# Kernel tuning notes

Hardware: AMD Instinct MI355X
Metric: run time of the kernel (lower is better)

Reference implementation:

```python
import jax, jax.numpy as jnp
import numpy as np

EPS = 1e-5

def _inorm(t, axes):
    m = t.mean(axis=axes, keepdims=True)
    v = t.var(axis=axes, keepdims=True)
    return (t - m) * jax.lax.rsqrt(v + EPS)

def setup_inputs() -> dict:
    key = jax.random.key(0)
    ks = jax.random.split(key, 7)
    b, c, d, o, h, w = 2, 128, 128, 128, 16, 16
    maxlen = 256
    return {
        "x": jax.random.normal(ks[0], (b, c, h, w), jnp.float32),
        "y": jax.random.normal(ks[1], (b, d, h, w), jnp.float32),
        "pos_emb": jax.random.normal(ks[2], (maxlen, c), jnp.float32) * 0.02,
        "w1": jax.random.normal(ks[3], (o, 2 * c + d), jnp.float32) * 0.05,
        "b1": jax.random.normal(ks[4], (o,), jnp.float32) * 0.01,
        "w2": jax.random.normal(ks[5], (o, o), jnp.float32) * 0.05,
        "b2": jax.random.normal(ks[6], (o,), jnp.float32) * 0.01,
    }

def reference(x, y, pos_emb, w1, b1, w2, b2):
    b, c, h, w = x.shape
    d = y.shape[1]
    hw = h * w
    # positional embedding: tokens = arange(hw), permute to channel-first
    pos = pos_emb[:hw].T.reshape(c, h, w)  # [c,h,w]
    x = x + pos[None]
    x = jax.nn.relu(_inorm(x, (2, 3)))
    y = jax.nn.relu(_inorm(y, (2, 3)))
    xf = x.reshape(b, c, hw)
    yf = y.reshape(b, d, hw)
    # conv1x1 over cat([x_i, x_j, y]) splits into three GEMMs (same math):
    Wi, Wj, Wy = w1[:, :c], w1[:, c:2 * c], w1[:, 2 * c:]
    A = jnp.einsum('oc,bcj->boj', Wi, xf)                    # varies along j
    B = jnp.einsum('oc,bci->boi', Wj, xf) + jnp.einsum('od,bdi->boi', Wy, yf)  # varies along i
    z = A[:, :, None, :] + B[:, :, :, None] + b1[None, :, None, None]  # [b,o,hw,hw]
    z = jax.nn.relu(_inorm(z, (2, 3)))
    # second conv1x1 then sum over dim=3 commutes: w2 @ sum_j z + hw*b2
    s = z.sum(axis=3)  # [b,o,hw]
    out = jnp.einsum('po,boi->bpi', w2, s) + hw * b2[None, :, None]
    return out.reshape(b, -1, h, w)
```

## Files before the change

### kernel.cpp

```cpp
#include <hip/hip_runtime.h>

#define HW 256
#define C  128

__device__ __forceinline__ void blockReduce4(float& a, float& b, float& c, float& d,
                                             float (*sm)[4]) {
    #pragma unroll
    for (int off = 32; off > 0; off >>= 1) {
        a += __shfl_down(a, off, 64);
        b += __shfl_down(b, off, 64);
        c += __shfl_down(c, off, 64);
        d += __shfl_down(d, off, 64);
    }
    const int wid  = threadIdx.x >> 6;
    const int lane = threadIdx.x & 63;
    if (lane == 0) { sm[wid][0] = a; sm[wid][1] = b; sm[wid][2] = c; sm[wid][3] = d; }
    __syncthreads();
    a = sm[0][0] + sm[1][0] + sm[2][0] + sm[3][0];
    b = sm[0][1] + sm[1][1] + sm[2][1] + sm[3][1];
    c = sm[0][2] + sm[1][2] + sm[2][2] + sm[3][2];
    d = sm[0][3] + sm[1][3] + sm[2][3] + sm[3][3];
}

__global__ __launch_bounds__(256) void k_norm(
        const float* __restrict__ x, const float* __restrict__ y,
        const float* __restrict__ pos, float* __restrict__ xn, float* __restrict__ yn) {
    __shared__ float sm[4][4];
    const int blk = blockIdx.x;
    const int tid = threadIdx.x;
    float v;
    float* dst;
    if (blk < 256) {
        const int c = blk & 127;
        v = x[blk * HW + tid] + pos[tid * C + c];
        dst = xn + blk * HW;
    } else {
        const int bc = blk - 256;
        v = y[bc * HW + tid];
        dst = yn + bc * HW;
    }
    float s = v, s2 = v * v, z3 = 0.0f, z4 = 0.0f;
    blockReduce4(s, s2, z3, z4, sm);
    const float m    = s  * (1.0f / 256.0f);
    const float var  = s2 * (1.0f / 256.0f) - m * m;
    const float r    = (v - m) * rsqrtf(var + 1e-5f);
    dst[tid] = r > 0.0f ? r : 0.0f;
}

__global__ __launch_bounds__(256) void k_rel(
        const float* __restrict__ xn, const float* __restrict__ yn,
        const float* __restrict__ w1, float* __restrict__ s_out) {
    __shared__ float sm[4][4];
    __shared__ float wrow[384];
    __shared__ float sha[256];
    const int bo = blockIdx.x;
    const int b  = bo >> 7;
    const int o  = bo & 127;
    const int i  = threadIdx.x;

    if (i < 128) {
        wrow[i]       = w1[o * 384 + i];
        wrow[128 + i] = w1[o * 384 + 128 + i];
        wrow[256 + i] = w1[o * 384 + 256 + i];
    }
    __syncthreads();

    const float* xb = xn + b * (C * HW);
    const float* yb = yn + b * (C * HW);

    float A = 0.0f, Bv = 0.0f;
    #pragma unroll 8
    for (int c = 0; c < 128; ++c) {
        const float xv = xb[c * HW + i];
        A  = fmaf(wrow[c],       xv, A);
        Bv = fmaf(wrow[128 + c], xv, Bv);
    }
    #pragma unroll 8
    for (int d2 = 0; d2 < 128; ++d2) {
        const float yv = yb[d2 * HW + i];
        Bv = fmaf(wrow[256 + d2], yv, Bv);
    }

    float sA = A, sA2 = A * A, sB = Bv, sB2 = Bv * Bv;
    blockReduce4(sA, sA2, sB, sB2, sm);

    const float mA   = sA  * (1.0f / 256.0f);
    const float mB   = sB  * (1.0f / 256.0f);
    const float varA = sA2 * (1.0f / 256.0f) - mA * mA;
    const float varB = sB2 * (1.0f / 256.0f) - mB * mB;
    const float istd = rsqrtf(varA + varB + 1e-5f);

    sha[i] = (A - mA) * istd;
    const float bb = (Bv - mB) * istd;
    __syncthreads();

    float acc = 0.0f;
    #pragma unroll 8
    for (int j = 0; j < 256; ++j) {
        const float t = sha[j] + bb;
        acc += (t > 0.0f ? t : 0.0f);
    }
    s_out[bo * HW + i] = acc;
}

__global__ __launch_bounds__(256) void k_out(
        const float* __restrict__ s_in, const float* __restrict__ w2,
        const float* __restrict__ b2, float* __restrict__ out) {
    __shared__ float wrow[128];
    const int bp = blockIdx.x;
    const int b  = bp >> 7;
    const int p  = bp & 127;
    const int i  = threadIdx.x;
    if (i < 128) wrow[i] = w2[p * 128 + i];
    __syncthreads();
    const float* sb = s_in + b * (C * HW);
    float acc = 256.0f * b2[p];
    #pragma unroll 8
    for (int o = 0; o < 128; ++o)
        acc = fmaf(wrow[o], sb[o * HW + i], acc);
    out[bp * HW + i] = acc;
}

extern "C" void kernel_launch(void* const* d_in, const int* in_sizes, int n_in,
                              void* d_out, int out_size, void* d_ws, size_t ws_size,
                              hipStream_t stream) {
    const float* x   = (const float*)d_in[0];
    const float* y   = (const float*)d_in[1];
    const float* pos = (const float*)d_in[2];
    const float* w1  = (const float*)d_in[3];
    const float* w2  = (const float*)d_in[5];
    const float* b2  = (const float*)d_in[6];
    float* out = (float*)d_out;

    float* xn = (float*)d_ws;
    float* yn = xn + 65536;
    float* s  = yn + 65536;

    k_norm<<<512, 256, 0, stream>>>(x, y, pos, xn, yn);
    k_rel <<<256, 256, 0, stream>>>(xn, yn, w1, s);
    k_out <<<256, 256, 0, stream>>>(s, w2, b2, out);
}
```

Baseline: 86.76 us.

## Split reductions across four thread groups in k_rel and k_out with 1024-thread blocks

k_rel and k_out now launch 1024 threads per block. Each quarter of the block handles a quarter of the channel reduction (and of the j-sum in k_rel), and the partial results are combined through shared memory. This shortens each thread's serial loop and raises the number of active waves, since only 256 blocks exist on a GPU with many CUs. The cost is extra shared-memory traffic, more barriers, and idle threads during the 256-wide phases. The block reduction now uses xor shuffles and is templated on the number of waves.

```diff
diff --git a/kernel.cpp b/kernel.cpp
--- a/kernel.cpp
+++ b/kernel.cpp
@@ -3,23 +3,26 @@
 #define HW 256
 #define C  128
 
+template<int NW>
 __device__ __forceinline__ void blockReduce4(float& a, float& b, float& c, float& d,
                                              float (*sm)[4]) {
     #pragma unroll
     for (int off = 32; off > 0; off >>= 1) {
-        a += __shfl_down(a, off, 64);
-        b += __shfl_down(b, off, 64);
-        c += __shfl_down(c, off, 64);
-        d += __shfl_down(d, off, 64);
+        a += __shfl_xor(a, off, 64);
+        b += __shfl_xor(b, off, 64);
+        c += __shfl_xor(c, off, 64);
+        d += __shfl_xor(d, off, 64);
     }
     const int wid  = threadIdx.x >> 6;
     const int lane = threadIdx.x & 63;
     if (lane == 0) { sm[wid][0] = a; sm[wid][1] = b; sm[wid][2] = c; sm[wid][3] = d; }
     __syncthreads();
-    a = sm[0][0] + sm[1][0] + sm[2][0] + sm[3][0];
-    b = sm[0][1] + sm[1][1] + sm[2][1] + sm[3][1];
-    c = sm[0][2] + sm[1][2] + sm[2][2] + sm[3][2];
-    d = sm[0][3] + sm[1][3] + sm[2][3] + sm[3][3];
+    a = 0.f; b = 0.f; c = 0.f; d = 0.f;
+    #pragma unroll
+    for (int w = 0; w < NW; ++w) {
+        a += sm[w][0]; b += sm[w][1]; c += sm[w][2]; d += sm[w][3];
+    }
+    __syncthreads();
 }
 
 __global__ __launch_bounds__(256) void k_norm(
@@ -39,50 +42,59 @@
         v = y[bc * HW + tid];
         dst = yn + bc * HW;
     }
-    float s = v, s2 = v * v, z3 = 0.0f, z4 = 0.0f;
-    blockReduce4(s, s2, z3, z4, sm);
-    const float m    = s  * (1.0f / 256.0f);
-    const float var  = s2 * (1.0f / 256.0f) - m * m;
-    const float r    = (v - m) * rsqrtf(var + 1e-5f);
+    float s = v, s2 = v * v, z3 = 0.f, z4 = 0.f;
+    blockReduce4<4>(s, s2, z3, z4, sm);
+    const float m   = s  * (1.0f / 256.0f);
+    const float var = s2 * (1.0f / 256.0f) - m * m;
+    const float r   = (v - m) * rsqrtf(var + 1e-5f);
     dst[tid] = r > 0.0f ? r : 0.0f;
 }
 
-__global__ __launch_bounds__(256) void k_rel(
+__global__ __launch_bounds__(1024) void k_rel(
         const float* __restrict__ xn, const float* __restrict__ yn,
         const float* __restrict__ w1, float* __restrict__ s_out) {
-    __shared__ float sm[4][4];
+    __shared__ float pA[4][256];
+    __shared__ float pB[4][256];
+    __shared__ float red[16][4];
+    __shared__ float aj[256];
+    __shared__ float bi[256];
     __shared__ float wrow[384];
-    __shared__ float sha[256];
+
+    const int t  = threadIdx.x;
+    const int i  = t & 255;
+    const int q  = t >> 8;
     const int bo = blockIdx.x;
     const int b  = bo >> 7;
     const int o  = bo & 127;
-    const int i  = threadIdx.x;
 
-    if (i < 128) {
-        wrow[i]       = w1[o * 384 + i];
-        wrow[128 + i] = w1[o * 384 + 128 + i];
-        wrow[256 + i] = w1[o * 384 + 256 + i];
-    }
+    if (t < 384) wrow[t] = w1[o * 384 + t];
     __syncthreads();
 
     const float* xb = xn + b * (C * HW);
     const float* yb = yn + b * (C * HW);
 
-    float A = 0.0f, Bv = 0.0f;
-    #pragma unroll 8
-    for (int c = 0; c < 128; ++c) {
+    float A = 0.f, Bv = 0.f;
+    const int c0 = q * 32;
+    #pragma unroll
+    for (int cc = 0; cc < 32; ++cc) {
+        const int c = c0 + cc;
         const float xv = xb[c * HW + i];
         A  = fmaf(wrow[c],       xv, A);
         Bv = fmaf(wrow[128 + c], xv, Bv);
+        const float yv = yb[c * HW + i];
+        Bv = fmaf(wrow[256 + c], yv, Bv);
     }
-    #pragma unroll 8
-    for (int d2 = 0; d2 < 128; ++d2) {
-        const float yv = yb[d2 * HW + i];
-        Bv = fmaf(wrow[256 + d2], yv, Bv);
+    pA[q][i] = A;
+    pB[q][i] = Bv;
+    __syncthreads();
+
+    float Af = 0.f, Bf = 0.f;
+    if (t < 256) {
+        Af = pA[0][i] + pA[1][i] + pA[2][i] + pA[3][i];
+        Bf = pB[0][i] + pB[1][i] + pB[2][i] + pB[3][i];
     }
-
-    float sA = A, sA2 = A * A, sB = Bv, sB2 = Bv * Bv;
-    blockReduce4(sA, sA2, sB, sB2, sm);
+    float sA = Af, sA2 = Af * Af, sB = Bf, sB2 = Bf * Bf;
+    blockReduce4<16>(sA, sA2, sB, sB2, red);
 
     const float mA   = sA  * (1.0f / 256.0f);
     const float mB   = sB  * (1.0f / 256.0f);
@@ -90,35 +102,50 @@
     const float varB = sB2 * (1.0f / 256.0f) - mB * mB;
     const float istd = rsqrtf(varA + varB + 1e-5f);
 
-    sha[i] = (A - mA) * istd;
-    const float bb = (Bv - mB) * istd;
+    if (t < 256) {
+        aj[i] = (Af - mA) * istd;
+        bi[i] = (Bf - mB) * istd;
+    }
     __syncthreads();
 
-    float acc = 0.0f;
-    #pragma unroll 8
-    for (int j = 0; j < 256; ++j) {
-        const float t = sha[j] + bb;
-        acc += (t > 0.0f ? t : 0.0f);
+    const float bb = bi[i];
+    float acc = 0.f;
+    const int j0 = q * 64;
+    #pragma unroll
+    for (int jj = 0; jj < 64; ++jj) {
+        const float v = aj[j0 + jj] + bb;
+        acc += (v > 0.f ? v : 0.f);
     }
-    s_out[bo * HW + i] = acc;
+    pA[q][i] = acc;
+    __syncthreads();
+    if (t < 256)
+        s_out[bo * HW + i] = pA[0][i] + pA[1][i] + pA[2][i] + pA[3][i];
 }
 
-__global__ __launch_bounds__(256) void k_out(
+__global__ __launch_bounds__(1024) void k_out(
         const float* __restrict__ s_in, const float* __restrict__ w2,
         const float* __restrict__ b2, float* __restrict__ out) {
     __shared__ float wrow[128];
+    __shared__ float pacc[4][256];
+    const int t  = threadIdx.x;
+    const int i  = t & 255;
+    const int q  = t >> 8;
     const int bp = blockIdx.x;
     const int b  = bp >> 7;
     const int p  = bp & 127;
-    const int i  = threadIdx.x;
-    if (i < 128) wrow[i] = w2[p * 128 + i];
+    if (t < 128) wrow[t] = w2[p * 128 + t];
     __syncthreads();
     const float* sb = s_in + b * (C * HW);
-    float acc = 256.0f * b2[p];
-    #pragma unroll 8
-    for (int o = 0; o < 128; ++o)
-        acc = fmaf(wrow[o], sb[o * HW + i], acc);
-    out[bp * HW + i] = acc;
+    float acc = 0.f;
+    const int o0 = q * 32;
+    #pragma unroll
+    for (int oo = 0; oo < 32; ++oo)
+        acc = fmaf(wrow[o0 + oo], sb[(o0 + oo) * HW + i], acc);
+    pacc[q][i] = acc;
+    __syncthreads();
+    if (t < 256)
+        out[bp * HW + i] = pacc[0][i] + pacc[1][i] + pacc[2][i] + pacc[3][i]
+                           + 256.0f * b2[p];
 }
 
 extern "C" void kernel_launch(void* const* d_in, const int* in_sizes, int n_in,
@@ -137,6 +164,6 @@
     float* s  = yn + 65536;
 
     k_norm<<<512, 256, 0, stream>>>(x, y, pos, xn, yn);
-    k_rel <<<256, 256, 0, stream>>>(xn, yn, w1, s);
-    k_out <<<256, 256, 0, stream>>>(s, w2, b2, out);
+    k_rel <<<256, 1024, 0, stream>>>(xn, yn, w1, s);
+    k_out <<<256, 1024, 0, stream>>>(s, w2, b2, out);
 }
```

Result: faster. 77.75 us (-10.4%).
